# Optimization experiments

Measured on AMD Instinct MI355X. Metric: run time of the kernel, lower is better.

## Reference

```python
import jax, jax.numpy as jnp
import numpy as np

N = 50000
E = 800000
IN_C = 128
OUT_C = 128
N_TYPES = 3
NEG_SLOPE = 0.2  # PyG GATConv default negative_slope


def setup_inputs() -> dict:
    key = jax.random.key(0)
    ks = jax.random.split(key, 10)
    x = jax.random.normal(ks[0], (N, IN_C), dtype=jnp.float32)
    edge_index = jax.random.randint(ks[1], (2, E), 0, N, dtype=jnp.int32)
    edge_type = jax.random.randint(ks[2], (E,), 0, N_TYPES, dtype=jnp.int32)
    node_type = jax.random.randint(ks[3], (N,), 0, 3, dtype=jnp.int32)
    s = 1.0 / np.sqrt(IN_C)
    emb_table = jax.random.normal(ks[4], (3, IN_C), dtype=jnp.float32)
    W = jax.random.normal(ks[5], (N_TYPES, IN_C, OUT_C), dtype=jnp.float32) * s
    att_src = jax.random.normal(ks[6], (N_TYPES, OUT_C), dtype=jnp.float32) * s
    att_dst = jax.random.normal(ks[7], (N_TYPES, OUT_C), dtype=jnp.float32) * s
    bias = jax.random.normal(ks[8], (N_TYPES, OUT_C), dtype=jnp.float32) * 0.01
    return {"x": x, "edge_index": edge_index, "edge_type": edge_type,
            "node_type": node_type, "emb_table": emb_table, "W": W,
            "att_src": att_src, "att_dst": att_dst, "bias": bias}


def reference(x, edge_index, edge_type, node_type, emb_table, W, att_src, att_dst, bias):
    # Eval mode: dropouts are identity. edge_index is non-empty -> GAT branch.
    n = x.shape[0]
    x = x + emb_table[node_type]  # node-type embedding add
    src, dst = edge_index[0], edge_index[1]
    out_sum = jnp.zeros((n, OUT_C), dtype=x.dtype)
    for t in range(N_TYPES):  # per-edge-type GATConv (heads=1, add_self_loops=True)
        xw = x @ W[t]                       # [N, out]
        a_s = xw @ att_src[t]               # [N] alpha_src per node
        a_d = xw @ att_dst[t]               # [N] alpha_dst per node
        mask = edge_type == t               # [E]
        e_raw = jax.nn.leaky_relu(a_s[src] + a_d[dst], NEG_SLOPE)  # [E]
        e_self = jax.nn.leaky_relu(a_s + a_d, NEG_SLOPE)           # [N] self-loop logit
        e_masked = jnp.where(mask, e_raw, -jnp.inf)
        m = jnp.maximum(jax.ops.segment_max(e_masked, dst, num_segments=n), e_self)
        m = jax.lax.stop_gradient(m)
        w_edge = jnp.where(mask, jnp.exp(e_raw - m[dst]), 0.0)     # [E]
        w_self = jnp.exp(e_self - m)                               # [N]
        denom = jax.ops.segment_sum(w_edge, dst, num_segments=n) + w_self
        num = jax.ops.segment_sum(w_edge[:, None] * xw[src], dst, num_segments=n) \
              + w_self[:, None] * xw
        out_sum = out_sum + num / denom[:, None] + bias[t]
        # (attention weights per type are w_edge/denom[dst]; only node output returned)
    return out_sum
```

## Files before the change

### kernel.cpp

```cpp
#include <hip/hip_runtime.h>
#include <math.h>

#define N_NODES 50000
#define N_EDGES 800000
#define C 128
#define NT 3
#define NEG 0.2f
#define CAP 64

#define GEMM_XB 782

#define NXCD 8
#define DST_PER_XCD (N_NODES / NXCD)
#define BIN_SLICES 256
#define EDGES_PER_SLICE (N_EDGES / BIN_SLICES)

typedef __attribute__((ext_vector_type(8))) short short8;
typedef __attribute__((ext_vector_type(4))) float f32x4;

__device__ __forceinline__ float leaky(float v) { return v > 0.f ? v : NEG * v; }

__device__ __forceinline__ unsigned short f2bf(float f) {
  unsigned int u = __float_as_uint(f);
  u = (u + 0x7FFFu + ((u >> 16) & 1u)) >> 16;
  return (unsigned short)u;
}
__device__ __forceinline__ float bf_lo(unsigned int w) { return __uint_as_float(w << 16); }
__device__ __forceinline__ float bf_hi(unsigned int w) { return __uint_as_float(w & 0xFFFF0000u); }

__global__ void k_prep(const float* __restrict__ W, unsigned short* __restrict__ Wt,
                       int* __restrict__ cnt) {
  int bid = blockIdx.x;
  if (bid < 192) {
    int idx = bid * 256 + threadIdx.x;
    int t = idx >> 14, rem = idx & 16383;
    int n = rem >> 7, k = rem & 127;
    Wt[((size_t)t * C + n) * C + k] = f2bf(W[((size_t)t * C + k) * C + n]);
  } else {
    int i4 = (bid - 192) * 256 + threadIdx.x;
    if (i4 < N_NODES / 4) ((int4*)cnt)[i4] = make_int4(0, 0, 0, 0);
  }
}

__global__ void k_bin(const int* __restrict__ ei, const int* __restrict__ etype,
                      int* __restrict__ cnt, int* __restrict__ buckets) {
  const int r = blockIdx.x & (NXCD - 1);
  const int slice = blockIdx.x >> 3;
  const int dlo = r * DST_PER_XCD, dhi = dlo + DST_PER_XCD;
  const int base = slice * EDGES_PER_SLICE;
  for (int i = threadIdx.x; i < EDGES_PER_SLICE; i += 256) {
    int e = base + i;
    int d = ei[N_EDGES + e];
    if (d >= dlo && d < dhi) {
      int s = ei[e];
      int t = etype[e];
      int p = atomicAdd(&cnt[d], 1);
      if (p < CAP) buckets[(size_t)d * CAP + p] = t * N_NODES + s;
    }
  }
}

__global__ void k_mm(const float* __restrict__ x, const int* __restrict__ node_type,
                     const float* __restrict__ emb, const unsigned short* __restrict__ Wt,
                     unsigned short* __restrict__ xwb,
                     const float* __restrict__ att_src, const float* __restrict__ att_dst,
                     float* __restrict__ a_s, float2* __restrict__ ad_es) {
  __shared__ unsigned short Bs[128][136];
  const int tid = threadIdx.x;
  const int gemm_id = blockIdx.x;
  const int t = gemm_id / GEMM_XB;
  const int rb = gemm_id - t * GEMM_XB;

  const int wid = tid >> 6, lane = tid & 63;
  const int m = lane & 15, quad = lane >> 4;
  const int row0 = rb * 64;
  const unsigned short* Wtt = Wt + (size_t)t * C * C;

  short8 af[4];
  {
    int arow = row0 + wid * 16 + m;
    bool valid = arow < N_NODES;
    const float* xr = x + (size_t)(valid ? arow : 0) * C;
    int nt = valid ? node_type[arow] : 0;
    const float* er = emb + nt * C;
#pragma unroll
    for (int k0i = 0; k0i < 4; ++k0i) {
      int cb = k0i * 32 + quad * 8;
      float4 v0 = *(const float4*)(xr + cb);
      float4 v1 = *(const float4*)(xr + cb + 4);
      float4 e0 = *(const float4*)(er + cb);
      float4 e1 = *(const float4*)(er + cb + 4);
      short8 f;
      f[0] = (short)f2bf(v0.x + e0.x);
      f[1] = (short)f2bf(v0.y + e0.y);
      f[2] = (short)f2bf(v0.z + e0.z);
      f[3] = (short)f2bf(v0.w + e0.w);
      f[4] = (short)f2bf(v1.x + e1.x);
      f[5] = (short)f2bf(v1.y + e1.y);
      f[6] = (short)f2bf(v1.z + e1.z);
      f[7] = (short)f2bf(v1.w + e1.w);
      af[k0i] = f;
    }
  }

#pragma unroll
  for (int it = 0; it < 8; ++it) {
    int c = tid + it * 256;
    int n = c >> 4, kc = c & 15;
    *(uint4*)&Bs[n][kc * 8] = *(const uint4*)(Wtt + (size_t)n * C + kc * 8);
  }
  __syncthreads();

  f32x4 acc[8] = {};
#pragma unroll
  for (int k0i = 0; k0i < 4; ++k0i) {
    int k0 = k0i * 32;
#pragma unroll
    for (int j = 0; j < 8; ++j) {
      short8 b = *(const short8*)&Bs[j * 16 + m][k0 + quad * 8];
      acc[j] = __builtin_amdgcn_mfma_f32_16x16x32_bf16(af[k0i], b, acc[j], 0, 0, 0);
    }
  }

  float ps[4] = {}, pd[4] = {};
#pragma unroll
  for (int j = 0; j < 8; ++j) {
    float as = att_src[t * C + j * 16 + m];
    float ad = att_dst[t * C + j * 16 + m];
#pragma unroll
    for (int reg = 0; reg < 4; ++reg) {
      int row = row0 + wid * 16 + quad * 4 + reg;
      float v = acc[j][reg];
      if (row < N_NODES) xwb[((size_t)t * N_NODES + row) * C + j * 16 + m] = f2bf(v);
      ps[reg] += v * as;
      pd[reg] += v * ad;
    }
  }
#pragma unroll
  for (int off = 1; off < 16; off <<= 1) {
#pragma unroll
    for (int reg = 0; reg < 4; ++reg) {
      ps[reg] += __shfl_xor(ps[reg], off);
      pd[reg] += __shfl_xor(pd[reg], off);
    }
  }
  if (m == 0) {
#pragma unroll
    for (int reg = 0; reg < 4; ++reg) {
      int row = row0 + wid * 16 + quad * 4 + reg;
      if (row < N_NODES) {
        int idx = t * N_NODES + row;
        a_s[idx] = ps[reg];
        ad_es[idx] = make_float2(pd[reg], leaky(ps[reg] + pd[reg]));
      }
    }
  }
}

__global__ void k_gather(const int* __restrict__ cnt, const int* __restrict__ buckets,
                         const unsigned short* __restrict__ xwb,
                         const float* __restrict__ a_s, const float2* __restrict__ ad_es,
                         const float* __restrict__ bias, float* __restrict__ out) {
  __shared__ float wcs[4][64];
  int wid = threadIdx.x >> 6;
  int lane = threadIdx.x & 63;
  int i = blockIdx.x * 4 + wid;
  int iu = __builtin_amdgcn_readfirstlane(i);
  const int* __restrict__ brow = buckets + (size_t)iu * CAP;
  int n = cnt[iu];
  if (n > CAP) n = CAP;

  int idxl = 0;
  if (lane < n) idxl = brow[lane];
  int tl = idxl >= 2 * N_NODES ? 2 : (idxl >= N_NODES ? 1 : 0);
  float as = a_s[idxl];
  float2 am = ad_es[tl * N_NODES + iu];
  float wl = (lane < n) ? __expf(leaky(as + am.x) - am.y) : 0.f;

  float s0 = tl == 0 ? wl : 0.f;
  float s1 = tl == 1 ? wl : 0.f;
  float s2 = tl == 2 ? wl : 0.f;
#pragma unroll
  for (int off = 1; off < 64; off <<= 1) {
    s0 += __shfl_xor(s0, off);
    s1 += __shfl_xor(s1, off);
    s2 += __shfl_xor(s2, off);
  }
  float inv3[NT] = {1.f / (s0 + 1.f), 1.f / (s1 + 1.f), 1.f / (s2 + 1.f)};
  wcs[wid][lane] = wl * inv3[tl];

  float acc0 = 0.f, acc1 = 0.f;
#pragma unroll
  for (int t = 0; t < NT; ++t) {
    int idx = t * N_NODES + iu;
    float coef = inv3[t];
    unsigned int w = ((const unsigned int*)(xwb + (size_t)idx * C))[lane];
    float2 b2 = ((const float2*)(bias + t * C))[lane];
    acc0 += coef * bf_lo(w) + b2.x;
    acc1 += coef * bf_hi(w) + b2.y;
  }

  const unsigned int* xwu = (const unsigned int*)xwb;
  int j = 0;
  for (; j + 16 <= n; j += 16) {
    float ac0 = 0.f, ac1 = 0.f;
#pragma unroll
    for (int k = 0; k < 16; ++k) {
      int idx = brow[j + k];
      float c = wcs[wid][j + k];
      unsigned int v = xwu[(size_t)idx * (C / 2) + lane];
      ac0 += c * bf_lo(v);
      ac1 += c * bf_hi(v);
    }
    acc0 += ac0; acc1 += ac1;
  }
  for (; j + 8 <= n; j += 8) {
    float ac0 = 0.f, ac1 = 0.f;
#pragma unroll
    for (int k = 0; k < 8; ++k) {
      int idx = brow[j + k];
      float c = wcs[wid][j + k];
      unsigned int v = xwu[(size_t)idx * (C / 2) + lane];
      ac0 += c * bf_lo(v);
      ac1 += c * bf_hi(v);
    }
    acc0 += ac0; acc1 += ac1;
  }
  for (; j < n; ++j) {
    int idx = brow[j];
    float c = wcs[wid][j];
    unsigned int v = xwu[(size_t)idx * (C / 2) + lane];
    acc0 += c * bf_lo(v);
    acc1 += c * bf_hi(v);
  }
  ((float2*)(out + (size_t)iu * C))[lane] = make_float2(acc0, acc1);
}

extern "C" void kernel_launch(void* const* d_in, const int* in_sizes, int n_in,
                              void* d_out, int out_size, void* d_ws, size_t ws_size,
                              hipStream_t stream) {
  const float* x       = (const float*)d_in[0];
  const int* edge_idx  = (const int*)d_in[1];
  const int* edge_type = (const int*)d_in[2];
  const int* node_type = (const int*)d_in[3];
  const float* emb     = (const float*)d_in[4];
  const float* W       = (const float*)d_in[5];
  const float* att_src = (const float*)d_in[6];
  const float* att_dst = (const float*)d_in[7];
  const float* bias    = (const float*)d_in[8];
  float* out = (float*)d_out;

  unsigned short* xwb = (unsigned short*)d_ws;
  unsigned short* Wt  = xwb + (size_t)NT * N_NODES * C;
  float*  a_s   = (float*)(Wt + (size_t)NT * C * C);
  float2* ad_es = (float2*)(a_s + (size_t)NT * N_NODES);
  int*    cnt   = (int*)(ad_es + (size_t)NT * N_NODES);
  int*    buckets = (int*)(cnt + N_NODES);

  k_prep<<<192 + 49, 256, 0, stream>>>(W, Wt, cnt);

  k_bin<<<NXCD * BIN_SLICES, 256, 0, stream>>>(edge_idx, edge_type, cnt, buckets);

  k_mm<<<NT * GEMM_XB, 256, 0, stream>>>(x, node_type, emb, Wt, xwb, att_src, att_dst,
                                         a_s, ad_es);

  k_gather<<<N_NODES / 4, 256, 0, stream>>>(cnt, buckets, xwb, a_s, ad_es, bias, out);
}
```

Measured before the change: 204.5 us.

## Fuse edge binning and GEMM into one interleaved kernel launch

Merges the edge-binning kernel and the per-type GEMM kernel into a single launch. Block ids are interleaved in groups of eight so binning blocks and GEMM blocks alternate, and the remaining GEMM blocks run after them. The intent is to overlap the atomic, memory-bound binning work with the MFMA GEMM work and to remove one kernel launch boundary. Binning blocks now reserve the GEMM's shared-memory allocation even though they do not use it, which can lower occupancy.

```diff
diff --git a/kernel.cpp b/kernel.cpp
--- a/kernel.cpp
+++ b/kernel.cpp
@@ -9,11 +9,15 @@
 #define CAP 64
 
 #define GEMM_XB 782
+#define MM_BLOCKS (NT * GEMM_XB)
 
 #define NXCD 8
 #define DST_PER_XCD (N_NODES / NXCD)
 #define BIN_SLICES 256
+#define BIN_BLOCKS (NXCD * BIN_SLICES)
 #define EDGES_PER_SLICE (N_EDGES / BIN_SLICES)
+
+#define BM_GRID (4096 + (MM_BLOCKS - 2048))
 
 typedef __attribute__((ext_vector_type(8))) short short8;
 typedef __attribute__((ext_vector_type(4))) float f32x4;
@@ -42,35 +46,42 @@
   }
 }
 
-__global__ void k_bin(const int* __restrict__ ei, const int* __restrict__ etype,
-                      int* __restrict__ cnt, int* __restrict__ buckets) {
-  const int r = blockIdx.x & (NXCD - 1);
-  const int slice = blockIdx.x >> 3;
-  const int dlo = r * DST_PER_XCD, dhi = dlo + DST_PER_XCD;
-  const int base = slice * EDGES_PER_SLICE;
-  for (int i = threadIdx.x; i < EDGES_PER_SLICE; i += 256) {
-    int e = base + i;
-    int d = ei[N_EDGES + e];
-    if (d >= dlo && d < dhi) {
-      int s = ei[e];
-      int t = etype[e];
-      int p = atomicAdd(&cnt[d], 1);
-      if (p < CAP) buckets[(size_t)d * CAP + p] = t * N_NODES + s;
-    }
-  }
-}
-
-__global__ void k_mm(const float* __restrict__ x, const int* __restrict__ node_type,
+__global__ void k_bm(const float* __restrict__ x, const int* __restrict__ node_type,
                      const float* __restrict__ emb, const unsigned short* __restrict__ Wt,
                      unsigned short* __restrict__ xwb,
                      const float* __restrict__ att_src, const float* __restrict__ att_dst,
-                     float* __restrict__ a_s, float2* __restrict__ ad_es) {
+                     float* __restrict__ a_s, float2* __restrict__ ad_es,
+                     const int* __restrict__ ei, const int* __restrict__ etype,
+                     int* __restrict__ cnt, int* __restrict__ buckets) {
   __shared__ unsigned short Bs[128][136];
+  const int bid = blockIdx.x;
   const int tid = threadIdx.x;
-  const int gemm_id = blockIdx.x;
-  const int t = gemm_id / GEMM_XB;
-  const int rb = gemm_id - t * GEMM_XB;
-
+
+  const int group = bid >> 3, inb = bid & 7;
+  int mm_sub;
+  if (group < 512) {
+    if ((group & 1) == 0) {
+      const int dlo = inb * DST_PER_XCD, dhi = dlo + DST_PER_XCD;
+      const int base = (group >> 1) * EDGES_PER_SLICE;
+      for (int i = tid; i < EDGES_PER_SLICE; i += 256) {
+        int e = base + i;
+        int d = ei[N_EDGES + e];
+        if (d >= dlo && d < dhi) {
+          int s = ei[e];
+          int t = etype[e];
+          int p = atomicAdd(&cnt[d], 1);
+          if (p < CAP) buckets[(size_t)d * CAP + p] = t * N_NODES + s;
+        }
+      }
+      return;
+    }
+    mm_sub = (group >> 1) * 8 + inb;
+  } else {
+    mm_sub = 2048 + (bid - 4096);
+  }
+
+  const int t = mm_sub / GEMM_XB;
+  const int rb = mm_sub - t * GEMM_XB;
   const int wid = tid >> 6, lane = tid & 63;
   const int m = lane & 15, quad = lane >> 4;
   const int row0 = rb * 64;
@@ -259,10 +270,8 @@
 
   k_prep<<<192 + 49, 256, 0, stream>>>(W, Wt, cnt);
 
-  k_bin<<<NXCD * BIN_SLICES, 256, 0, stream>>>(edge_idx, edge_type, cnt, buckets);
-
-  k_mm<<<NT * GEMM_XB, 256, 0, stream>>>(x, node_type, emb, Wt, xwb, att_src, att_dst,
-                                         a_s, ad_es);
+  k_bm<<<BM_GRID, 256, 0, stream>>>(x, node_type, emb, Wt, xwb, att_src, att_dst,
+                                    a_s, ad_es, edge_idx, edge_type, cnt, buckets);
 
   k_gather<<<N_NODES / 4, 256, 0, stream>>>(cnt, buckets, xwb, a_s, ad_es, bias, out);
 }
```

Measured after the change: 209.0 us. 2.2% more time.
